# Performance work log

Measured on AMD Instinct MI355X. Metric: run time of the kernel, lower is better.

Reference implementation:

```python
import jax, jax.numpy as jnp
import numpy as np


def setup_inputs() -> dict:
    key = jax.random.key(0)
    ks = jax.random.split(key, 6)
    B, H, N, C, O, G = 4, 24, 512, 120, 512, 5
    x = jax.random.normal(ks[0], (B, H, N, C), dtype=jnp.float32)
    t_indices = jnp.arange(H, dtype=jnp.int64)
    time_emb = jax.random.normal(ks[1], (H, 8), dtype=jnp.float32)
    # kaiming-uniform-ish init for base linear weight
    fan_in = C + 8
    bound = float(np.sqrt(6.0 / fan_in))
    base_w = jax.random.uniform(ks[2], (O, C + 8), minval=-bound, maxval=bound, dtype=jnp.float32)
    base_b = jax.random.uniform(ks[3], (O,), minval=-1.0 / np.sqrt(fan_in), maxval=1.0 / np.sqrt(fan_in), dtype=jnp.float32)
    spline_weight = jax.random.uniform(ks[4], (O, C + 8, G), minval=-0.1, maxval=0.1, dtype=jnp.float32)
    return {"x": x, "t_indices": t_indices, "time_emb": time_emb,
            "base_w": base_w, "base_b": base_b, "spline_weight": spline_weight}


def reference(x, t_indices, time_emb, base_w, base_b, spline_weight):
    B, H, N, C = x.shape
    G = spline_weight.shape[-1]
    grid = jnp.linspace(-1.0, 1.0, G, dtype=x.dtype)  # non-trainable buffer
    # time embedding lookup, broadcast over batch and nodes: [B,H,N,8]
    t_emb = jnp.broadcast_to(time_emb[t_indices][None, :, None, :], (B, H, N, time_emb.shape[-1]))
    x_in = jnp.concatenate([x, t_emb], axis=-1)  # [B,H,N,C+8]
    # base path: SiLU then linear
    base = jnp.einsum('bhni,oi->bhno', jax.nn.silu(x_in), base_w) + base_b
    # RBF basis: [B,H,N,C+8,G]
    inv_h = (G - 1) / 2.0  # 1 / (2/(G-1))
    basis = jnp.exp(-(((x_in[..., None] - grid) * inv_h) ** 2))
    spline = jnp.einsum('bhnig,oig->bhno', basis, spline_weight)
    return base + spline
```

## Files before the change

### kernel.cpp

```cpp
#include <hip/hip_runtime.h>
#include <hip/hip_bf16.h>

typedef __attribute__((ext_vector_type(4))) float f32x4;
typedef __attribute__((ext_vector_type(8))) short bf16x8;

#define GLDS16(gp, lp) __builtin_amdgcn_global_load_lds( \
    (__attribute__((address_space(1))) void*)(void*)(gp), \
    (__attribute__((address_space(3))) void*)(lp), 16, 0, 0)

static constexpr int Mtot = 49152;
static constexpr int Otot = 512;
static constexpr int Hh   = 24;

__device__ inline unsigned short f2bf(float f) {
    __hip_bfloat16 h = __float2bfloat16(f);
    unsigned short u;
    __builtin_memcpy(&u, &h, 2);
    return u;
}

__global__ __launch_bounds__(256) void prep_W(
        const float* __restrict__ bw, const float* __restrict__ sw,
        uint4* __restrict__ Wt)
{
    int tid = blockIdx.x * 256 + threadIdx.x;
    int p    = tid & 15;
    int o    = (tid >> 4) & 511;
    int iter = tid >> 13;
    int ck = p ^ (o & 7);
    unsigned u[4] = {0u, 0u, 0u, 0u};
    if (ck < 12) {
        unsigned short s[8];
        #pragma unroll
        for (int e = 0; e < 8; ++e) {
            int k = iter * 96 + ck * 8 + e;
            int i = k / 6, f = k - i * 6;
            float v = (f == 0) ? bw[o * 128 + i] : sw[(o * 128 + i) * 5 + (f - 1)];
            s[e] = f2bf(v);
        }
        #pragma unroll
        for (int n = 0; n < 4; ++n) u[n] = s[2 * n] | ((unsigned)s[2 * n + 1] << 16);
    }
    Wt[tid] = make_uint4(u[0], u[1], u[2], u[3]);
}

__global__ __launch_bounds__(256, 2) void gemm_kan(
        const float* __restrict__ x, const int* __restrict__ t_idx,
        const float* __restrict__ temb,
        const char* __restrict__ Wt,
        const float* __restrict__ bias,
        float* __restrict__ out)
{
    __shared__ char AsB[128 * 256];
    __shared__ char BsB[128 * 256];
    const int t    = threadIdx.x;
    const int wave = t >> 6;
    const int lane = t & 63;
    const int m_base = blockIdx.x * 128;
    const int n_base = blockIdx.y * 128;
    const int wm = (wave >> 1) * 64;
    const int wn = (wave & 1) * 64;
    const int ll = lane & 15;
    const int q4 = lane >> 4;

    f32x4 acc[4][4] = {};

    const char* bsrc0 = Wt + (size_t)n_base * 256 + t * 16;
    char* ldsB = BsB + wave * 1024;

    const int row = t >> 1;
    const int oct = t & 1;
    const int ht  = t_idx[(m_base >> 9) % Hh];
    const float* xrow = x + (size_t)(m_base + row) * 120;
    const float* trow = temb + ht * 8;

    float4 xa, xb;
    {
        const int i0 = 8 * oct;
        xa = *(const float4*)(xrow + i0);
        xb = *(const float4*)(xrow + i0 + 4);
    }

    for (int it = 0; it < 8; ++it) {
        const char* bsrc = bsrc0 + (size_t)it * (512 * 256);
        #pragma unroll
        for (int q = 0; q < 8; ++q)
            GLDS16(bsrc + q * 4096, ldsB + q * 4096);

        float v[8];
        v[0] = xa.x; v[1] = xa.y; v[2] = xa.z; v[3] = xa.w;
        v[4] = xb.x; v[5] = xb.y; v[6] = xb.z; v[7] = xb.w;

        if (it < 7) {
            const int i0 = (it + 1) * 16 + 8 * oct;
            const float* p = (i0 < 120) ? (xrow + i0) : (trow + (i0 - 120));
            xa = *(const float4*)p;
            xb = *(const float4*)(p + 4);
        }

        unsigned short s[48];
        #pragma unroll
        for (int c = 0; c < 8; ++c) {
            const float vv = v[c];
            s[c * 6 + 0] = f2bf(vv * __builtin_amdgcn_rcpf(1.0f + __expf(-vv)));
            #pragma unroll
            for (int g = 0; g < 5; ++g) {
                const float d = 2.0f * (vv - (-1.0f + 0.5f * g));
                s[c * 6 + 1 + g] = f2bf(__expf(-d * d));
            }
        }
        #pragma unroll
        for (int j = 0; j < 6; ++j) {
            const int ck = 6 * oct + j;
            const int phys = ck ^ (row & 7);
            unsigned u[4];
            #pragma unroll
            for (int n = 0; n < 4; ++n)
                u[n] = s[j * 8 + 2 * n] | ((unsigned)s[j * 8 + 2 * n + 1] << 16);
            *(uint4*)(AsB + row * 256 + phys * 16) = make_uint4(u[0], u[1], u[2], u[3]);
        }
        __syncthreads();

        #pragma unroll
        for (int kk = 0; kk < 3; ++kk) {
            bf16x8 af[4], bf[4];
            #pragma unroll
            for (int mi = 0; mi < 4; ++mi) {
                const int r = wm + mi * 16 + ll;
                af[mi] = *(const bf16x8*)(AsB + r * 256 + (((kk * 4 + q4) ^ (ll & 7)) * 16));
            }
            #pragma unroll
            for (int ni = 0; ni < 4; ++ni) {
                const int r = wn + ni * 16 + ll;
                bf[ni] = *(const bf16x8*)(BsB + r * 256 + (((kk * 4 + q4) ^ (ll & 7)) * 16));
            }
            #pragma unroll
            for (int mi = 0; mi < 4; ++mi)
                #pragma unroll
                for (int ni = 0; ni < 4; ++ni)
                    acc[mi][ni] = __builtin_amdgcn_mfma_f32_16x16x32_bf16(
                        af[mi], bf[ni], acc[mi][ni], 0, 0, 0);
        }
        __syncthreads();
    }

    const int col0 = n_base + wn + ll;
    const int row0 = m_base + wm + q4 * 4;
    #pragma unroll
    for (int ni = 0; ni < 4; ++ni) {
        const int col = col0 + ni * 16;
        const float bv = bias[col];
        #pragma unroll
        for (int mi = 0; mi < 4; ++mi) {
            #pragma unroll
            for (int r = 0; r < 4; ++r) {
                out[(long)(row0 + mi * 16 + r) * Otot + col] = acc[mi][ni][r] + bv;
            }
        }
    }
}

extern "C" void kernel_launch(void* const* d_in, const int* in_sizes, int n_in,
                              void* d_out, int out_size, void* d_ws, size_t ws_size,
                              hipStream_t stream) {
    const float* x    = (const float*)d_in[0];
    const int*   tidx = (const int*)  d_in[1];
    const float* temb = (const float*)d_in[2];
    const float* bw   = (const float*)d_in[3];
    const float* bb   = (const float*)d_in[4];
    const float* sw   = (const float*)d_in[5];
    float* out = (float*)d_out;

    char* Wt = (char*)d_ws;

    prep_W<<<65536 / 256, 256, 0, stream>>>(bw, sw, (uint4*)Wt);
    gemm_kan<<<dim3(Mtot / 128, Otot / 128), 256, 0, stream>>>(
        x, tidx, temb, Wt, bb, out);
}
```

Measured before the change: 174.9 us.

## Compute full output width per block to avoid recomputing RBF basis across N tiles

Each block now covers all 512 output columns with 512 threads, so the SiLU and RBF basis features for a row tile are computed once instead of once per column tile. The K dimension is reordered by feature type (base, then each grid point), and the weights are packed to match in a k-major layout without padding. B tiles are double-buffered through direct global-to-LDS loads, and the next A chunk is generated in registers one step ahead. The costs are more registers per thread (a 4x8 accumulator tile), a larger LDS footprint, an extra barrier per iteration, and the loss of the XOR swizzle, which may cause LDS bank conflicts.

New measurement: 180.3 us. 1.03x slower.

```diff
diff --git a/kernel.cpp b/kernel.cpp
--- a/kernel.cpp
+++ b/kernel.cpp
@@ -19,142 +19,162 @@
     return u;
 }
 
+__device__ inline uint4 gen8(const int f, const float4 a, const float4 b) {
+    float v[8] = {a.x, a.y, a.z, a.w, b.x, b.y, b.z, b.w};
+    unsigned short s[8];
+    if (f == 0) {
+        #pragma unroll
+        for (int e = 0; e < 8; ++e)
+            s[e] = f2bf(v[e] * __builtin_amdgcn_rcpf(1.0f + __expf(-v[e])));
+    } else {
+        const float cg = -1.0f + 0.5f * (float)(f - 1);
+        #pragma unroll
+        for (int e = 0; e < 8; ++e) {
+            const float d = 2.0f * (v[e] - cg);
+            s[e] = f2bf(__expf(-d * d));
+        }
+    }
+    uint4 u;
+    u.x = s[0] | ((unsigned)s[1] << 16);
+    u.y = s[2] | ((unsigned)s[3] << 16);
+    u.z = s[4] | ((unsigned)s[5] << 16);
+    u.w = s[6] | ((unsigned)s[7] << 16);
+    return u;
+}
+
 __global__ __launch_bounds__(256) void prep_W(
         const float* __restrict__ bw, const float* __restrict__ sw,
         uint4* __restrict__ Wt)
 {
-    int tid = blockIdx.x * 256 + threadIdx.x;
-    int p    = tid & 15;
-    int o    = (tid >> 4) & 511;
-    int iter = tid >> 13;
-    int ck = p ^ (o & 7);
-    unsigned u[4] = {0u, 0u, 0u, 0u};
-    if (ck < 12) {
-        unsigned short s[8];
+    const int tid = blockIdx.x * 256 + threadIdx.x;
+    const int col = tid & 511;
+    const int C   = tid >> 9;
+    const int f   = C >> 4;
+    const int i0  = (C & 15) * 8;
+    unsigned short s[8];
+    if (f == 0) {
+        const float4 a = *(const float4*)(bw + col * 128 + i0);
+        const float4 b = *(const float4*)(bw + col * 128 + i0 + 4);
+        const float v[8] = {a.x, a.y, a.z, a.w, b.x, b.y, b.z, b.w};
         #pragma unroll
-        for (int e = 0; e < 8; ++e) {
-            int k = iter * 96 + ck * 8 + e;
-            int i = k / 6, f = k - i * 6;
-            float v = (f == 0) ? bw[o * 128 + i] : sw[(o * 128 + i) * 5 + (f - 1)];
-            s[e] = f2bf(v);
-        }
+        for (int e = 0; e < 8; ++e) s[e] = f2bf(v[e]);
+    } else {
         #pragma unroll
-        for (int n = 0; n < 4; ++n) u[n] = s[2 * n] | ((unsigned)s[2 * n + 1] << 16);
+        for (int e = 0; e < 8; ++e)
+            s[e] = f2bf(sw[(col * 128 + i0 + e) * 5 + (f - 1)]);
     }
-    Wt[tid] = make_uint4(u[0], u[1], u[2], u[3]);
+    uint4 u;
+    u.x = s[0] | ((unsigned)s[1] << 16);
+    u.y = s[2] | ((unsigned)s[3] << 16);
+    u.z = s[4] | ((unsigned)s[5] << 16);
+    u.w = s[6] | ((unsigned)s[7] << 16);
+    Wt[tid] = u;
 }
 
-__global__ __launch_bounds__(256, 2) void gemm_kan(
+__global__ __launch_bounds__(512, 2) void gemm_kan(
         const float* __restrict__ x, const int* __restrict__ t_idx,
         const float* __restrict__ temb,
         const char* __restrict__ Wt,
         const float* __restrict__ bias,
         float* __restrict__ out)
 {
-    __shared__ char AsB[128 * 256];
-    __shared__ char BsB[128 * 256];
+    __shared__ char Alds[8 * 128 * 16];
+    __shared__ char Blds[2][8 * 512 * 16];
+
     const int t    = threadIdx.x;
     const int wave = t >> 6;
     const int lane = t & 63;
+    const int ll   = lane & 15;
+    const int q4   = lane >> 4;
+    const int wm   = (wave >> 2) * 64;
+    const int wn   = (wave & 3) * 128;
     const int m_base = blockIdx.x * 128;
-    const int n_base = blockIdx.y * 128;
-    const int wm = (wave >> 1) * 64;
-    const int wn = (wave & 1) * 64;
-    const int ll = lane & 15;
-    const int q4 = lane >> 4;
 
-    f32x4 acc[4][4] = {};
-
-    const char* bsrc0 = Wt + (size_t)n_base * 256 + t * 16;
-    char* ldsB = BsB + wave * 1024;
-
-    const int row = t >> 1;
-    const int oct = t & 1;
+    const int row = t >> 2;
+    const int cp  = t & 3;
     const int ht  = t_idx[(m_base >> 9) % Hh];
     const float* xrow = x + (size_t)(m_base + row) * 120;
     const float* trow = temb + ht * 8;
 
-    float4 xa, xb;
-    {
-        const int i0 = 8 * oct;
-        xa = *(const float4*)(xrow + i0);
-        xb = *(const float4*)(xrow + i0 + 4);
+    float4 xc[4][2];
+    #pragma unroll
+    for (int g = 0; g < 4; ++g) {
+        const int i0 = ((g & 1) * 8 + cp + (g >> 1) * 4) * 8;
+        const float* p = (i0 < 120) ? (xrow + i0) : (trow + (i0 - 120));
+        xc[g][0] = *(const float4*)p;
+        xc[g][1] = *(const float4*)(p + 4);
     }
 
-    for (int it = 0; it < 8; ++it) {
-        const char* bsrc = bsrc0 + (size_t)it * (512 * 256);
+    f32x4 acc[4][8] = {};
+
+    auto stageB = [&](int it, int buf) {
+        const char* src = Wt + ((size_t)((it * 8 + wave) * 512 + lane) << 4);
+        char* dst = &Blds[buf][wave * 8192];
         #pragma unroll
         for (int q = 0; q < 8; ++q)
-            GLDS16(bsrc + q * 4096, ldsB + q * 4096);
+            GLDS16(src + (q << 10), dst + (q << 10));
+    };
 
-        float v[8];
-        v[0] = xa.x; v[1] = xa.y; v[2] = xa.z; v[3] = xa.w;
-        v[4] = xb.x; v[5] = xb.y; v[6] = xb.z; v[7] = xb.w;
+    stageB(0, 0);
+    {
+        uint4 a0 = gen8(0, xc[0][0], xc[0][1]);
+        uint4 a1 = gen8(0, xc[2][0], xc[2][1]);
+        *(uint4*)(Alds + (((cp    ) * 128 + row) << 4)) = a0;
+        *(uint4*)(Alds + (((cp + 4) * 128 + row) << 4)) = a1;
+    }
+    uint4 p0 = gen8(0, xc[1][0], xc[1][1]);
+    uint4 p1 = gen8(0, xc[3][0], xc[3][1]);
+    __syncthreads();
 
-        if (it < 7) {
-            const int i0 = (it + 1) * 16 + 8 * oct;
-            const float* p = (i0 < 120) ? (xrow + i0) : (trow + (i0 - 120));
-            xa = *(const float4*)p;
-            xb = *(const float4*)(p + 4);
+    #pragma unroll
+    for (int it = 0; it < 12; ++it) {
+        if (it + 1 < 12) stageB(it + 1, (it + 1) & 1);
+
+        uint4 n0 = {}, n1 = {};
+        if (it + 2 < 12) {
+            const int f = (it + 2) >> 1, h = (it + 2) & 1;
+            n0 = gen8(f, xc[h][0],     xc[h][1]);
+            n1 = gen8(f, xc[2 + h][0], xc[2 + h][1]);
         }
 
-        unsigned short s[48];
+        const char* B = Blds[it & 1];
         #pragma unroll
-        for (int c = 0; c < 8; ++c) {
-            const float vv = v[c];
-            s[c * 6 + 0] = f2bf(vv * __builtin_amdgcn_rcpf(1.0f + __expf(-vv)));
+        for (int kk = 0; kk < 2; ++kk) {
+            const int ch = kk * 4 + q4;
+            bf16x8 af[4], bf[8];
             #pragma unroll
-            for (int g = 0; g < 5; ++g) {
-                const float d = 2.0f * (vv - (-1.0f + 0.5f * g));
-                s[c * 6 + 1 + g] = f2bf(__expf(-d * d));
-            }
-        }
-        #pragma unroll
-        for (int j = 0; j < 6; ++j) {
-            const int ck = 6 * oct + j;
-            const int phys = ck ^ (row & 7);
-            unsigned u[4];
+            for (int mi = 0; mi < 4; ++mi)
+                af[mi] = *(const bf16x8*)(Alds + ((ch * 128 + wm + mi * 16 + ll) << 4));
             #pragma unroll
-            for (int n = 0; n < 4; ++n)
-                u[n] = s[j * 8 + 2 * n] | ((unsigned)s[j * 8 + 2 * n + 1] << 16);
-            *(uint4*)(AsB + row * 256 + phys * 16) = make_uint4(u[0], u[1], u[2], u[3]);
-        }
-        __syncthreads();
-
-        #pragma unroll
-        for (int kk = 0; kk < 3; ++kk) {
-            bf16x8 af[4], bf[4];
-            #pragma unroll
-            for (int mi = 0; mi < 4; ++mi) {
-                const int r = wm + mi * 16 + ll;
-                af[mi] = *(const bf16x8*)(AsB + r * 256 + (((kk * 4 + q4) ^ (ll & 7)) * 16));
-            }
-            #pragma unroll
-            for (int ni = 0; ni < 4; ++ni) {
-                const int r = wn + ni * 16 + ll;
-                bf[ni] = *(const bf16x8*)(BsB + r * 256 + (((kk * 4 + q4) ^ (ll & 7)) * 16));
-            }
+            for (int ni = 0; ni < 8; ++ni)
+                bf[ni] = *(const bf16x8*)(B + ((ch * 512 + wn + ni * 16 + ll) << 4));
             #pragma unroll
             for (int mi = 0; mi < 4; ++mi)
                 #pragma unroll
-                for (int ni = 0; ni < 4; ++ni)
+                for (int ni = 0; ni < 8; ++ni)
                     acc[mi][ni] = __builtin_amdgcn_mfma_f32_16x16x32_bf16(
                         af[mi], bf[ni], acc[mi][ni], 0, 0, 0);
         }
         __syncthreads();
+        if (it + 1 < 12) {
+            *(uint4*)(Alds + (((cp    ) * 128 + row) << 4)) = p0;
+            *(uint4*)(Alds + (((cp + 4) * 128 + row) << 4)) = p1;
+            p0 = n0; p1 = n1;
+        }
+        __syncthreads();
     }
 
-    const int col0 = n_base + wn + ll;
+    const int col0 = wn + ll;
     const int row0 = m_base + wm + q4 * 4;
     #pragma unroll
-    for (int ni = 0; ni < 4; ++ni) {
+    for (int ni = 0; ni < 8; ++ni) {
         const int col = col0 + ni * 16;
         const float bv = bias[col];
         #pragma unroll
         for (int mi = 0; mi < 4; ++mi) {
             #pragma unroll
             for (int r = 0; r < 4; ++r) {
-                out[(long)(row0 + mi * 16 + r) * Otot + col] = acc[mi][ni][r] + bv;
+                out[(size_t)(row0 + mi * 16 + r) * Otot + col] = acc[mi][ni][r] + bv;
             }
         }
     }
@@ -173,7 +193,6 @@
 
     char* Wt = (char*)d_ws;
 
-    prep_W<<<65536 / 256, 256, 0, stream>>>(bw, sw, (uint4*)Wt);
-    gemm_kan<<<dim3(Mtot / 128, Otot / 128), 256, 0, stream>>>(
-        x, tidx, temb, Wt, bb, out);
+    prep_W<<<49152 / 256, 256, 0, stream>>>(bw, sw, (uint4*)Wt);
+    gemm_kan<<<Mtot / 128, 512, 0, stream>>>(x, tidx, temb, Wt, bb, out);
 }
```

## Retile GEMM to 64x256 with per-wave column strips and factor RBF exponentials

Applied to the files above, without the earlier changes.

The block tile changes from 128x128 to 64x256: each wave now owns a 64-column strip of the output across all 64 rows, and the grid is reordered so N varies fastest. With 64 rows per block, the per-thread activation work (SiLU plus RBF features) drops to 4 channels. The five Gaussian RBF values are now built from two exponentials, exp(-4v^2) and exp(4v), plus a reciprocal and constant multiplies, instead of five separate exps. The aim is to cut transcendental work and redundant activation computation. The cost is more B tile data per block, possible overflow in exp(4v) for large inputs, and a changed LDS footprint (80KB).

Result: faster. 171.1 us (-2.2%).

```diff
diff --git a/kernel.cpp b/kernel.cpp
--- a/kernel.cpp
+++ b/kernel.cpp
@@ -51,67 +51,66 @@
         const float* __restrict__ bias,
         float* __restrict__ out)
 {
-    __shared__ char AsB[128 * 256];
-    __shared__ char BsB[128 * 256];
+    __shared__ char AsB[64 * 256];
+    __shared__ char BsB[256 * 256];
     const int t    = threadIdx.x;
     const int wave = t >> 6;
     const int lane = t & 63;
-    const int m_base = blockIdx.x * 128;
-    const int n_base = blockIdx.y * 128;
-    const int wm = (wave >> 1) * 64;
-    const int wn = (wave & 1) * 64;
-    const int ll = lane & 15;
-    const int q4 = lane >> 4;
+    const int ll   = lane & 15;
+    const int q4   = lane >> 4;
+    const int wn   = wave * 64;
+    const int m_base = blockIdx.y * 64;
+    const int n_base = blockIdx.x * 256;
 
     f32x4 acc[4][4] = {};
 
-    const char* bsrc0 = Wt + (size_t)n_base * 256 + t * 16;
-    char* ldsB = BsB + wave * 1024;
+    const char* bsrc0 = Wt + (size_t)(n_base + wn) * 256 + lane * 16;
+    char* ldsB = BsB + wn * 256;
 
-    const int row = t >> 1;
-    const int oct = t & 1;
+    const int row = t >> 2;
+    const int q   = t & 3;
     const int ht  = t_idx[(m_base >> 9) % Hh];
     const float* xrow = x + (size_t)(m_base + row) * 120;
     const float* trow = temb + ht * 8;
 
-    float4 xa, xb;
-    {
-        const int i0 = 8 * oct;
-        xa = *(const float4*)(xrow + i0);
-        xb = *(const float4*)(xrow + i0 + 4);
-    }
+    auto chanptr = [&](int i0) -> const float* {
+        return (i0 < 120) ? (xrow + i0) : (trow + (i0 - 120));
+    };
 
+    float4 xv = *(const float4*)chanptr(4 * q);
+
+    constexpr float C1 = 0.36787944117f;
+    constexpr float C4 = 0.01831563889f;
+
+    #pragma unroll
     for (int it = 0; it < 8; ++it) {
         const char* bsrc = bsrc0 + (size_t)it * (512 * 256);
         #pragma unroll
-        for (int q = 0; q < 8; ++q)
-            GLDS16(bsrc + q * 4096, ldsB + q * 4096);
+        for (int p = 0; p < 16; ++p)
+            GLDS16(bsrc + p * 1024, ldsB + p * 1024);
 
-        float v[8];
-        v[0] = xa.x; v[1] = xa.y; v[2] = xa.z; v[3] = xa.w;
-        v[4] = xb.x; v[5] = xb.y; v[6] = xb.z; v[7] = xb.w;
+        const float4 cur = xv;
+        if (it < 7) xv = *(const float4*)chanptr((it + 1) * 16 + 4 * q);
 
-        if (it < 7) {
-            const int i0 = (it + 1) * 16 + 8 * oct;
-            const float* p = (i0 < 120) ? (xrow + i0) : (trow + (i0 - 120));
-            xa = *(const float4*)p;
-            xb = *(const float4*)(p + 4);
-        }
-
-        unsigned short s[48];
+        float v[4] = {cur.x, cur.y, cur.z, cur.w};
+        unsigned short s[24];
         #pragma unroll
-        for (int c = 0; c < 8; ++c) {
+        for (int c = 0; c < 4; ++c) {
             const float vv = v[c];
             s[c * 6 + 0] = f2bf(vv * __builtin_amdgcn_rcpf(1.0f + __expf(-vv)));
-            #pragma unroll
-            for (int g = 0; g < 5; ++g) {
-                const float d = 2.0f * (vv - (-1.0f + 0.5f * g));
-                s[c * 6 + 1 + g] = f2bf(__expf(-d * d));
-            }
+            const float tt = __expf(-4.0f * vv * vv);
+            const float uu = __expf(4.0f * vv);
+            const float rr = __builtin_amdgcn_rcpf(uu);
+            const float tu = tt * uu, tr = tt * rr;
+            s[c * 6 + 1] = f2bf(tr * rr * C4);
+            s[c * 6 + 2] = f2bf(tr * C1);
+            s[c * 6 + 3] = f2bf(tt);
+            s[c * 6 + 4] = f2bf(tu * C1);
+            s[c * 6 + 5] = f2bf(tu * uu * C4);
         }
         #pragma unroll
-        for (int j = 0; j < 6; ++j) {
-            const int ck = 6 * oct + j;
+        for (int j = 0; j < 3; ++j) {
+            const int ck = 3 * q + j;
             const int phys = ck ^ (row & 7);
             unsigned u[4];
             #pragma unroll
@@ -126,7 +125,7 @@
             bf16x8 af[4], bf[4];
             #pragma unroll
             for (int mi = 0; mi < 4; ++mi) {
-                const int r = wm + mi * 16 + ll;
+                const int r = mi * 16 + ll;
                 af[mi] = *(const bf16x8*)(AsB + r * 256 + (((kk * 4 + q4) ^ (ll & 7)) * 16));
             }
             #pragma unroll
@@ -145,7 +144,7 @@
     }
 
     const int col0 = n_base + wn + ll;
-    const int row0 = m_base + wm + q4 * 4;
+    const int row0 = m_base + q4 * 4;
     #pragma unroll
     for (int ni = 0; ni < 4; ++ni) {
         const int col = col0 + ni * 16;
@@ -174,6 +173,6 @@
     char* Wt = (char*)d_ws;
 
     prep_W<<<65536 / 256, 256, 0, stream>>>(bw, sw, (uint4*)Wt);
-    gemm_kan<<<dim3(Mtot / 128, Otot / 128), 256, 0, stream>>>(
+    gemm_kan<<<dim3(Otot / 256, Mtot / 64), 256, 0, stream>>>(
         x, tidx, temb, Wt, bb, out);
 }
```
